# Kernel optimization log

Measured on AMD Instinct MI355X. Metric: run time of the kernel, lower is better.

Reference implementation:

```python
import jax, jax.numpy as jnp
import numpy as np

B, N, ND, H = 8, 1024, 64, 128
NUM_OPS, NUM_PARAMS, SKETCH = 64, 256, 128


def setup_inputs() -> dict:
    key = jax.random.key(0)
    ks = iter(jax.random.split(key, 64))

    def rn(shape, s=0.05):
        return jax.random.normal(next(ks), shape, dtype=jnp.float32) * s

    inp = {
        'node_features': jax.random.normal(next(ks), (B, N, ND), dtype=jnp.float32),
        'adjacency': (jax.random.uniform(next(ks), (B, N, N)) < 0.05).astype(jnp.float32),
        'mask': jnp.ones((B, N), jnp.float32),
    }
    for name, din in (('g1', ND), ('g2', H), ('g3', H)):
        inp[name + '_W'] = rn((din, H))
        inp[name + '_b'] = jnp.zeros((H,), jnp.float32)
        inp[name + '_aW'] = rn((2 * H,))
        inp[name + '_ab'] = jnp.zeros((), jnp.float32)
    for l in (0, 1):
        inp[f'l{l}_Wih'] = rn((4 * H, H))
        inp[f'l{l}_Whh'] = rn((4 * H, H))
        inp[f'l{l}_bih'] = jnp.zeros((4 * H,), jnp.float32)
        inp[f'l{l}_bhh'] = jnp.zeros((4 * H,), jnp.float32)
    for name, dout in (('op', NUM_OPS), ('pa', NUM_PARAMS), ('sk', SKETCH), ('no', ND)):
        inp[name + '_W1'] = rn((H, H))
        inp[name + '_b1'] = jnp.zeros((H,), jnp.float32)
        inp[name + '_W2'] = rn((H, dout))
        inp[name + '_b2'] = jnp.zeros((dout,), jnp.float32)
    return inp


def _gnn(x, adj, W, b, aW, ab):
    # h = Linear(x); att[b,i,j] = sigmoid(aW . [h_j ; h_i] + ab)  (cat order from the torch code)
    h = x @ W + b                      # [B,N,H]
    D = W.shape[1]
    sj = h @ aW[:D]                    # contribution of the dim-1-expanded term (h_j)
    si = h @ aW[D:]                    # contribution of the dim-2-expanded term (h_i)
    att = jax.nn.sigmoid(si[:, :, None] + sj[:, None, :] + ab) * adj  # [B,N,N]
    return jnp.einsum('bij,bjd->bid', att, h)


def _lstm(x, Wih, Whh, bih, bhh):
    # single torch-style LSTM layer, gate order i,f,g,o; zero initial state
    Bx, Hh = x.shape[0], Whh.shape[1]

    def step(carry, xt):
        h, c = carry
        g = xt @ Wih.T + h @ Whh.T + (bih + bhh)       # [B,4H]
        i, f, gg, o = jnp.split(g, 4, axis=-1)
        c = jax.nn.sigmoid(f) * c + jax.nn.sigmoid(i) * jnp.tanh(gg)
        h = jax.nn.sigmoid(o) * jnp.tanh(c)
        return (h, c), h

    z = jnp.zeros((Bx, Hh), x.dtype)
    _, ys = jax.lax.scan(step, (z, z), jnp.swapaxes(x, 0, 1))
    return jnp.swapaxes(ys, 0, 1)


def _mlp(x, W1, b1, W2, b2):
    return jax.nn.relu(x @ W1 + b1) @ W2 + b2


def reference(node_features, adjacency, mask,
              g1_W, g1_b, g1_aW, g1_ab,
              g2_W, g2_b, g2_aW, g2_ab,
              g3_W, g3_b, g3_aW, g3_ab,
              l0_Wih, l0_Whh, l0_bih, l0_bhh,
              l1_Wih, l1_Whh, l1_bih, l1_bhh,
              op_W1, op_b1, op_W2, op_b2,
              pa_W1, pa_b1, pa_W2, pa_b2,
              sk_W1, sk_b1, sk_W2, sk_b2,
              no_W1, no_b1, no_W2, no_b2):
    h = jax.nn.relu(_gnn(node_features, adjacency, g1_W, g1_b, g1_aW, g1_ab))
    h = jax.nn.relu(_gnn(h, adjacency, g2_W, g2_b, g2_aW, g2_ab))
    h = _gnn(h, adjacency, g3_W, g3_b, g3_aW, g3_ab)
    lo = _lstm(h, l0_Wih, l0_Whh, l0_bih, l0_bhh)
    lo = _lstm(lo, l1_Wih, l1_Whh, l1_bih, l1_bhh)
    op_pred = _mlp(lo, op_W1, op_b1, op_W2, op_b2)
    param_pred = _mlp(lo, pa_W1, pa_b1, pa_W2, pa_b2)
    sketch_pred = _mlp(lo, sk_W1, sk_b1, sk_W2, sk_b2)
    node_pred = _mlp(h, no_W1, no_b1, no_W2, no_b2)
    return (op_pred, param_pred, sketch_pred, node_pred)
```

## Files before the change

### kernel.cpp

```cpp
#include <hip/hip_runtime.h>

typedef __attribute__((ext_vector_type(8))) short short8;
typedef __attribute__((ext_vector_type(4))) float f32x4;
typedef __attribute__((ext_vector_type(2))) unsigned int u32x2;

__device__ __forceinline__ unsigned short bf16_of(float f) {
    unsigned u = __builtin_bit_cast(unsigned, f);
    u += 0x7fffu + ((u >> 16) & 1u);
    return (unsigned short)(u >> 16);
}
__device__ __forceinline__ unsigned bf16pk(float a, float b) {
    return (unsigned)bf16_of(a) | ((unsigned)bf16_of(b) << 16);
}
__device__ __forceinline__ float fexp2(float x) { return __builtin_amdgcn_exp2f(x); }
__device__ __forceinline__ float frcp(float x) { return __builtin_amdgcn_rcpf(x); }
__device__ __forceinline__ float sigm(float x) { return frcp(1.f + fexp2(-1.44269504f * x)); }
__device__ __forceinline__ f32x4 mfma16(short8 a, short8 b, f32x4 c) {
    return __builtin_amdgcn_mfma_f32_16x16x32_bf16(a, b, c, 0, 0, 0);
}
__device__ __forceinline__ float dpp_shr8(float x) {
    return __builtin_bit_cast(float, __builtin_amdgcn_update_dpp(
        0, __builtin_bit_cast(int, x), 0x118, 0xF, 0xF, true));
}
__device__ __forceinline__ float dpp_shl8(float x) {
    return __builtin_bit_cast(float, __builtin_amdgcn_update_dpp(
        0, __builtin_bit_cast(int, x), 0x108, 0xF, 0xF, true));
}

__global__ __launch_bounds__(256) void gemm_f32(
    const float* __restrict__ A, const float* __restrict__ B,
    const float* __restrict__ bias, float* __restrict__ C,
    int M, int N, int K, int BT, int RELU, int PACK)
{
    __shared__ float As[64][33];
    __shared__ float Bs[32][68];
    const int tid = threadIdx.x;
    const int tx = tid & 15, ty = tid >> 4;
    const int m0 = blockIdx.y * 64, n0 = blockIdx.x * 64;
    float acc[4][4];
#pragma unroll
    for (int i = 0; i < 4; ++i)
#pragma unroll
        for (int j = 0; j < 4; ++j) acc[i][j] = 0.f;

    for (int k0 = 0; k0 < K; k0 += 32) {
        __syncthreads();
        {
            const int r = tid >> 2, kk = (tid & 3) * 8;
            const float* src = A + (size_t)(m0 + r) * K + k0 + kk;
            f32x4 v0 = *(const f32x4*)src;
            f32x4 v1 = *(const f32x4*)(src + 4);
#pragma unroll
            for (int e = 0; e < 4; ++e) { As[r][kk + e] = v0[e]; As[r][kk + 4 + e] = v1[e]; }
        }
        if (!BT) {
            const int kk = tid >> 3, nn = (tid & 7) * 8;
            const float* src = B + (size_t)(k0 + kk) * N + n0 + nn;
            f32x4 v0 = *(const f32x4*)src;
            f32x4 v1 = *(const f32x4*)(src + 4);
#pragma unroll
            for (int e = 0; e < 4; ++e) { Bs[kk][nn + e] = v0[e]; Bs[kk][nn + 4 + e] = v1[e]; }
        } else {
            const int n = tid >> 2, kk = (tid & 3) * 8;
            const float* src = B + (size_t)(n0 + n) * K + k0 + kk;
            f32x4 v0 = *(const f32x4*)src;
            f32x4 v1 = *(const f32x4*)(src + 4);
#pragma unroll
            for (int e = 0; e < 4; ++e) { Bs[kk + e][n] = v0[e]; Bs[kk + 4 + e][n] = v1[e]; }
        }
        __syncthreads();
#pragma unroll 8
        for (int k = 0; k < 32; ++k) {
            float a0 = As[ty * 4 + 0][k], a1 = As[ty * 4 + 1][k];
            float a2 = As[ty * 4 + 2][k], a3 = As[ty * 4 + 3][k];
            f32x4 bv = *(const f32x4*)&Bs[k][tx * 4];
#pragma unroll
            for (int j = 0; j < 4; ++j) {
                acc[0][j] += a0 * bv[j]; acc[1][j] += a1 * bv[j];
                acc[2][j] += a2 * bv[j]; acc[3][j] += a3 * bv[j];
            }
        }
    }
    f32x4 bv = {};
    if (bias != nullptr) bv = *(const f32x4*)&bias[n0 + tx * 4];
#pragma unroll
    for (int i = 0; i < 4; ++i) {
        f32x4 res = {};
#pragma unroll
        for (int j = 0; j < 4; ++j) {
            float v = acc[i][j] + bv[j];
            if (RELU) v = fmaxf(v, 0.f);
            res[j] = v;
        }
        const int m = m0 + ty * 4 + i;
        if (!PACK) {
            *(f32x4*)&C[(size_t)m * N + n0 + tx * 4] = res;
        } else {
            const int b = m >> 10, t = m & 1023;
            const int n = n0 + tx * 4;
            const int pr = n >> 7, h = n & 127;
            if (pr == 3) {
#pragma unroll
                for (int j = 0; j < 4; ++j) res[j] *= 0.5f;
            }
            *(f32x4*)&C[(((size_t)t * 4 + pr) * 8 + b) * 128 + h] = res;
        }
    }
}

__global__ __launch_bounds__(256) void gemm_gnn(
    const float* __restrict__ A, const float* __restrict__ B,
    const float* __restrict__ bias, const float* __restrict__ aW,
    unsigned short* __restrict__ hT, float* __restrict__ siP,
    float* __restrict__ sjP, int K)
{
    __shared__ float As[64][33];
    __shared__ float Bs[32][68];
    __shared__ unsigned short T[64][70];
    const int tid = threadIdx.x;
    const int tx = tid & 15, ty = tid >> 4;
    const int m0 = blockIdx.y * 64, n0 = blockIdx.x * 64;
    float acc[4][4];
#pragma unroll
    for (int i = 0; i < 4; ++i)
#pragma unroll
        for (int j = 0; j < 4; ++j) acc[i][j] = 0.f;

    for (int k0 = 0; k0 < K; k0 += 32) {
        __syncthreads();
        {
            const int r = tid >> 2, kk = (tid & 3) * 8;
            const float* src = A + (size_t)(m0 + r) * K + k0 + kk;
            f32x4 v0 = *(const f32x4*)src;
            f32x4 v1 = *(const f32x4*)(src + 4);
#pragma unroll
            for (int e = 0; e < 4; ++e) { As[r][kk + e] = v0[e]; As[r][kk + 4 + e] = v1[e]; }
        }
        {
            const int kk = tid >> 3, nn = (tid & 7) * 8;
            const float* src = B + (size_t)(k0 + kk) * 128 + n0 + nn;
            f32x4 v0 = *(const f32x4*)src;
            f32x4 v1 = *(const f32x4*)(src + 4);
#pragma unroll
            for (int e = 0; e < 4; ++e) { Bs[kk][nn + e] = v0[e]; Bs[kk][nn + 4 + e] = v1[e]; }
        }
        __syncthreads();
#pragma unroll 8
        for (int k = 0; k < 32; ++k) {
            float a0 = As[ty * 4 + 0][k], a1 = As[ty * 4 + 1][k];
            float a2 = As[ty * 4 + 2][k], a3 = As[ty * 4 + 3][k];
            f32x4 bv = *(const f32x4*)&Bs[k][tx * 4];
#pragma unroll
            for (int j = 0; j < 4; ++j) {
                acc[0][j] += a0 * bv[j]; acc[1][j] += a1 * bv[j];
                acc[2][j] += a2 * bv[j]; acc[3][j] += a3 * bv[j];
            }
        }
    }
    f32x4 bv = *(const f32x4*)&bias[n0 + tx * 4];
#pragma unroll
    for (int i = 0; i < 4; ++i)
#pragma unroll
        for (int j = 0; j < 4; ++j) acc[i][j] += bv[j];

    f32x4 wj = *(const f32x4*)&aW[n0 + tx * 4];
    f32x4 wi = *(const f32x4*)&aW[128 + n0 + tx * 4];
#pragma unroll
    for (int i = 0; i < 4; ++i) {
        float pj = acc[i][0] * wj[0] + acc[i][1] * wj[1] + acc[i][2] * wj[2] + acc[i][3] * wj[3];
        float pi = acc[i][0] * wi[0] + acc[i][1] * wi[1] + acc[i][2] * wi[2] + acc[i][3] * wi[3];
#pragma unroll
        for (int o = 8; o > 0; o >>= 1) {
            pj += __shfl_xor(pj, o);
            pi += __shfl_xor(pi, o);
        }
        if (tx == 0) {
            const int m = m0 + ty * 4 + i;
            sjP[blockIdx.x * 8192 + m] = pj;
            siP[blockIdx.x * 8192 + m] = pi;
        }
    }

#pragma unroll
    for (int i = 0; i < 4; ++i) {
        unsigned* tp = (unsigned*)&T[ty * 4 + i][tx * 4];
        tp[0] = bf16pk(acc[i][0], acc[i][1]);
        tp[1] = bf16pk(acc[i][2], acc[i][3]);
    }
    __syncthreads();
    const int b = m0 >> 10, node0 = m0 & 1023;
    const int r = tid >> 4, c4 = (tid & 15) * 4;
#pragma unroll
    for (int rr = 0; rr < 4; ++rr) {
        const int d = rr * 16 + r;
        u32x2 o;
        o[0] = (unsigned)T[c4 + 0][d] | ((unsigned)T[c4 + 1][d] << 16);
        o[1] = (unsigned)T[c4 + 2][d] | ((unsigned)T[c4 + 3][d] << 16);
        *(u32x2*)(hT + ((size_t)b * 128 + n0 + d) * 1024 + node0 + c4) = o;
    }
}

__global__ __launch_bounds__(256) void gnn_agg(
    const float* __restrict__ adj, const unsigned short* __restrict__ hT,
    const float* __restrict__ siP, const float* __restrict__ sjP,
    const float* __restrict__ abp, float* __restrict__ out, int RELU)
{
    __shared__ __align__(16) unsigned short Alds[32 * 40];
    __shared__ __align__(16) unsigned short Blds[128 * 40];
    __shared__ float sjL[1024];
    const int b = blockIdx.y, it = blockIdx.x;
    const int i0 = it * 32;
    const int tid = threadIdx.x, lane = tid & 63, w = tid >> 6;
    const int quad = lane >> 4, col = lane & 15;
    const int rh = w & 1, nh = w >> 1;
    const float ab = abp[0];
    const float* adjb = adj + (size_t)b * 1024 * 1024;
    const unsigned short* hTb = hT + (size_t)b * 128 * 1024;

    for (int j = tid; j < 1024; j += 256)
        sjL[j] = sjP[b * 1024 + j] + sjP[8192 + b * 1024 + j];

    const int ar_ = tid >> 3, ash = (tid & 7) * 4;
    const int br_ = tid >> 1, bsh = (tid & 1) * 16;
    const float sii = siP[b * 1024 + i0 + ar_] + siP[8192 + b * 1024 + i0 + ar_] + ab;

    const float* aptr = adjb + (size_t)(i0 + ar_) * 1024 + ash;
    const unsigned short* bptr = hTb + (size_t)br_ * 1024 + bsh;

    f32x4 paA = *(const f32x4*)(aptr);
    short8 pbA0 = *(const short8*)(bptr);
    short8 pbA1 = *(const short8*)(bptr + 8);
    f32x4 paB = *(const f32x4*)(aptr + 32);
    short8 pbB0 = *(const short8*)(bptr + 32);
    short8 pbB1 = *(const short8*)(bptr + 40);

    f32x4 acc[4] = {};

    for (int j0 = 0; j0 < 1024; j0 += 64) {
        __syncthreads();
        {
            float s0 = sigm(sii + sjL[j0 + ash + 0]) * paA[0];
            float s1 = sigm(sii + sjL[j0 + ash + 1]) * paA[1];
            float s2 = sigm(sii + sjL[j0 + ash + 2]) * paA[2];
            float s3 = sigm(sii + sjL[j0 + ash + 3]) * paA[3];
            u32x2 o = {bf16pk(s0, s1), bf16pk(s2, s3)};
            *(u32x2*)&Alds[ar_ * 40 + ash] = o;
            *(short8*)&Blds[br_ * 40 + bsh] = pbA0;
            *(short8*)&Blds[br_ * 40 + bsh + 8] = pbA1;
        }
        if (j0 + 64 < 1024) {
            paA = *(const f32x4*)(aptr + j0 + 64);
            pbA0 = *(const short8*)(bptr + j0 + 64);
            pbA1 = *(const short8*)(bptr + j0 + 72);
        }
        __syncthreads();
        {
            short8 af = *(const short8*)&Alds[(rh * 16 + col) * 40 + quad * 8];
#pragma unroll
            for (int nt = 0; nt < 4; ++nt) {
                short8 bf = *(const short8*)&Blds[((nh * 4 + nt) * 16 + col) * 40 + quad * 8];
                acc[nt] = mfma16(af, bf, acc[nt]);
            }
        }
        __syncthreads();
        {
            float s0 = sigm(sii + sjL[j0 + 32 + ash + 0]) * paB[0];
            float s1 = sigm(sii + sjL[j0 + 32 + ash + 1]) * paB[1];
            float s2 = sigm(sii + sjL[j0 + 32 + ash + 2]) * paB[2];
            float s3 = sigm(sii + sjL[j0 + 32 + ash + 3]) * paB[3];
            u32x2 o = {bf16pk(s0, s1), bf16pk(s2, s3)};
            *(u32x2*)&Alds[ar_ * 40 + ash] = o;
            *(short8*)&Blds[br_ * 40 + bsh] = pbB0;
            *(short8*)&Blds[br_ * 40 + bsh + 8] = pbB1;
        }
        if (j0 + 96 < 1024) {
            paB = *(const f32x4*)(aptr + j0 + 96);
            pbB0 = *(const short8*)(bptr + j0 + 96);
            pbB1 = *(const short8*)(bptr + j0 + 104);
        }
        __syncthreads();
        {
            short8 af = *(const short8*)&Alds[(rh * 16 + col) * 40 + quad * 8];
#pragma unroll
            for (int nt = 0; nt < 4; ++nt) {
                short8 bf = *(const short8*)&Blds[((nh * 4 + nt) * 16 + col) * 40 + quad * 8];
                acc[nt] = mfma16(af, bf, acc[nt]);
            }
        }
    }
    const int ibase = i0 + rh * 16 + quad * 4;
#pragma unroll
    for (int nt = 0; nt < 4; ++nt) {
        const int d = (nh * 4 + nt) * 16 + col;
#pragma unroll
        for (int r = 0; r < 4; ++r) {
            float v = acc[nt][r];
            if (RELU) v = fmaxf(v, 0.f);
            out[((size_t)b * 1024 + ibase + r) * 128 + d] = v;
        }
    }
}

struct PrepArgs {
    const float* src[8];
    unsigned short* dst[8];
    int N[8];
};
__global__ __launch_bounds__(256) void prep_k(
    PrepArgs pa, const float* bih0, const float* bhh0,
    float* bsum, int* flags)
{
    const int m = blockIdx.x;
    const int tid = threadIdx.x;
    if (m < 8) {
        const float* src = pa.src[m];
        unsigned short* dst = pa.dst[m];
        const int N = pa.N[m];
        const int n0 = tid >> 4, kc = (tid & 15) * 8;
        for (int n = n0; n < N; n += 16) {
            unsigned o[4];
#pragma unroll
            for (int e = 0; e < 8; e += 2)
                o[e >> 1] = bf16pk(src[(size_t)(kc + e) * N + n],
                                   src[(size_t)(kc + e + 1) * N + n]);
            *(u32x2*)&dst[n * 128 + kc] = *(u32x2*)&o[0];
            *(u32x2*)&dst[n * 128 + kc + 4] = *(u32x2*)&o[2];
        }
    } else {
        bsum[tid] = bih0[tid] + bhh0[tid];
        bsum[tid + 256] = bih0[tid + 256] + bhh0[tid + 256];
        if (tid < 3) flags[tid] = 0;
    }
}


struct HeadArgs {
    const unsigned short* W1T[4];
    const float* b1[4];
    const unsigned short* W2T[4];
    const float* b2[4];
    float* outp[4];
};

__device__ __forceinline__ void lstm_epilogue(
    const f32x4 accs[4], f32x4 xv0, f32x4 xv1, float* cst, float* hv,
    bool lo, float selLo)
{
    float t0[4], t1[4];
#pragma unroll
    for (int i = 0; i < 4; ++i) {
        float P0 = (lo ? accs[0][i] : dpp_shr8(accs[1][i])) + xv0[i];
        float P1 = (lo ? accs[2][i] : dpp_shr8(accs[3][i])) + xv1[i];
        P1 = fmaxf(P1, -30.f);
        t0[i] = frcp(1.f + fexp2(-1.44269504f * P0));
        float u = fexp2(-2.88539008f * P1);
        t1[i] = (1.f - selLo * u) * frcp(1.f + u);
    }
    float c2[4], og[4];
#pragma unroll
    for (int i = 0; i < 4; ++i) {
        float ig = t0[i];
        float fg = dpp_shl8(t0[i]);
        float gg = t1[i];
        og[i] = dpp_shl8(t1[i]);
        c2[i] = fg * cst[i] + ig * gg;
        cst[i] = c2[i];
    }
    float pc0 = lo ? c2[0] : dpp_shr8(c2[1]);
    float pc1 = lo ? c2[2] : dpp_shr8(c2[3]);
    pc0 = fmaxf(pc0, -30.f);
    pc1 = fmaxf(pc1, -30.f);
    float u0 = fexp2(-2.88539008f * pc0);
    float tc0 = (1.f - u0) * frcp(1.f + u0);
    float u1 = fexp2(-2.88539008f * pc1);
    float tc1 = (1.f - u1) * frcp(1.f + u1);
    float th[4] = {tc0, dpp_shl8(tc0), tc1, dpp_shl8(tc1)};
#pragma unroll
    for (int i = 0; i < 4; ++i) hv[i] = og[i] * th[i];
}

template <int SINK>
__device__ __forceinline__ void lstm_step(
    unsigned short* Hc, unsigned short* Hn, const short8 afr[4][4],
    f32x4 xv0, f32x4 xv1, float* cst, unsigned short* __restrict__ sink,
    int t, int col, int quad, int h4, int b)
{
    short8 bfr[4];
#pragma unroll
    for (int c = 0; c < 4; ++c)
        bfr[c] = *(const short8*)&Hc[col * 136 + c * 32 + quad * 8];
    f32x4 accs[4] = {};
#pragma unroll
    for (int c = 0; c < 4; ++c)
#pragma unroll
        for (int g = 0; g < 4; ++g)
            accs[g] = mfma16(afr[g][c], bfr[c], accs[g]);

    const bool lo = (col < 8);
    const float selLo = lo ? 1.f : 0.f;
    float hv[4];
    lstm_epilogue(accs, xv0, xv1, cst, hv, lo, selLo);
    if (lo) {
        u32x2 hb = {bf16pk(hv[0], hv[1]), bf16pk(hv[2], hv[3])};
        *(u32x2*)&Hn[b * 136 + h4] = hb;
        if (SINK == 0)
            *(u32x2*)(sink + (size_t)t * 1024 + b * 128 + h4) = hb;
        else
            *(u32x2*)(sink + ((size_t)t * 8 + b) * 128 + h4) = hb;
    }
    __builtin_amdgcn_s_waitcnt(0xC07F);
    __builtin_amdgcn_s_barrier();
}

template <int A32, int LROWS>
__device__ void head_strip(
    const void* __restrict__ Asrc, int row0,
    const unsigned short* __restrict__ W1T, const float* __restrict__ b1,
    const unsigned short* __restrict__ W2T, const float* __restrict__ b2,
    float* __restrict__ outp, int dout, unsigned short* A2, int tid)
{
    const int lane = tid & 63, w = tid >> 6;
    const int quad = lane >> 4, col = lane & 15;
    const int mrow = w * 16 + col;
    f32x4 acc[8] = {};
#pragma unroll
    for (int kc = 0; kc < 4; ++kc) {
        short8 af;
        if (A32) {
            const float* s = (const float*)Asrc + (size_t)(row0 + mrow) * 128 + kc * 32 + quad * 8;
            f32x4 v0 = *(const f32x4*)s, v1 = *(const f32x4*)(s + 4);
            short8 v;
#pragma unroll
            for (int j = 0; j < 4; ++j) {
                v[j] = (short)bf16_of(v0[j]);
                v[4 + j] = (short)bf16_of(v1[j]);
            }
            af = v;
        } else {
            af = *(const short8*)((const unsigned short*)Asrc +
                                  (size_t)(row0 + mrow) * 128 + kc * 32 + quad * 8);
        }
#pragma unroll
        for (int nt = 0; nt < 8; ++nt) {
            short8 bf = *(const short8*)&W1T[(nt * 16 + col) * 128 + kc * 32 + quad * 8];
            acc[nt] = mfma16(af, bf, acc[nt]);
        }
    }
    float b1v[8];
#pragma unroll
    for (int nt = 0; nt < 8; ++nt) b1v[nt] = b1[nt * 16 + col];
    __syncthreads();
#pragma unroll
    for (int nt = 0; nt < 8; ++nt)
#pragma unroll
        for (int i = 0; i < 4; ++i) {
            const int mm = w * 16 + quad * 4 + i;
            A2[mm * 136 + nt * 16 + col] = bf16_of(fmaxf(acc[nt][i] + b1v[nt], 0.f));
        }
    __syncthreads();
    const int ntiles = dout >> 4;
    for (int np = 0; np < ntiles; np += 8) {
        const int nts = (ntiles - np < 8) ? ntiles - np : 8;
        f32x4 acc2[8] = {};
#pragma unroll
        for (int kc = 0; kc < 4; ++kc) {
            short8 a2f = *(const short8*)&A2[mrow * 136 + kc * 32 + quad * 8];
            for (int nt = 0; nt < nts; ++nt) {
                short8 bf = *(const short8*)&W2T[((np + nt) * 16 + col) * 128 + kc * 32 + quad * 8];
                acc2[nt] = mfma16(a2f, bf, acc2[nt]);
            }
        }
        for (int nt = 0; nt < nts; ++nt) {
            const int n = (np + nt) * 16 + col;
            const float bb = b2[n];
#pragma unroll
            for (int i = 0; i < 4; ++i) {
                const int r = row0 + w * 16 + quad * 4 + i;
                size_t off;
                if (LROWS) off = ((size_t)(r & 7) * 1024 + (r >> 3)) * dout + n;
                else       off = (size_t)r * dout + n;
                outp[off] = acc2[nt][i] + bb;
            }
        }
    }
}

__global__ __launch_bounds__(512) void lstm_pipe(
    const float* __restrict__ xw0, const float* __restrict__ Whh0,
    const float* __restrict__ Wih1, const float* __restrict__ Whh1,
    const float* __restrict__ bih1, const float* __restrict__ bhh1,
    unsigned short* __restrict__ hbuf, float* __restrict__ xw1,
    int* __restrict__ flags, unsigned short* __restrict__ out1b,
    const float* __restrict__ bufH3, HeadArgs ha)
{
    __shared__ __align__(16) unsigned short H[2][16 * 136];
    __shared__ __align__(16) unsigned short A2[128 * 136];
    const int tid = threadIdx.x;
    const int lane = tid & 63;
    const int w = tid >> 6;
    const int quad = lane >> 4;
    const int col = lane & 15;
    const int b = col & 7;
    const int prA = col >> 3;
    const int h4 = w * 16 + quad * 4;

    if (blockIdx.x >= 3) {
        const int wid = blockIdx.x - 3;
        for (int s = wid; s < 64; s += 8)
            head_strip<1, 0>(bufH3, s * 128, ha.W1T[3], ha.b1[3],
                             ha.W2T[3], ha.b2[3], ha.outp[3], 64, A2, tid);
        for (int s = wid; s < 64; s += 8) {
            if (tid == 0) {
                while (__hip_atomic_load(&flags[2], __ATOMIC_ACQUIRE,
                                         __HIP_MEMORY_SCOPE_AGENT) < s + 1)
                    __builtin_amdgcn_s_sleep(16);
            }
            __syncthreads();
            head_strip<0, 1>(out1b, s * 128, ha.W1T[0], ha.b1[0],
                             ha.W2T[0], ha.b2[0], ha.outp[0], 64, A2, tid);
            head_strip<0, 1>(out1b, s * 128, ha.W1T[1], ha.b1[1],
                             ha.W2T[1], ha.b2[1], ha.outp[1], 256, A2, tid);
            head_strip<0, 1>(out1b, s * 128, ha.W1T[2], ha.b1[2],
                             ha.W2T[2], ha.b2[2], ha.outp[2], 128, A2, tid);
        }
        return;
    }

    if (blockIdx.x == 1) {
        short8 afrI[4][4];
        f32x4 biasv[4];
#pragma unroll
        for (int g = 0; g < 4; ++g) {
            const float gsc = (g == 3) ? 0.5f : 1.f;
            const int row = g * 128 + w * 16 + col;
#pragma unroll
            for (int c = 0; c < 4; ++c) {
                const float* src = Wih1 + row * 128 + c * 32 + quad * 8;
                short8 v;
#pragma unroll
                for (int j = 0; j < 8; ++j) v[j] = (short)bf16_of(src[j] * gsc);
                afrI[g][c] = v;
            }
            const int rb = g * 128 + w * 16 + quad * 4;
            f32x4 b1 = *(const f32x4*)&bih1[rb];
            f32x4 b2 = *(const f32x4*)&bhh1[rb];
#pragma unroll
            for (int e = 0; e < 4; ++e) biasv[g][e] = (b1[e] + b2[e]) * gsc;
        }
        for (int k = 0; k < 64; ++k) {
            if (tid == 0) {
                while (__hip_atomic_load(&flags[0], __ATOMIC_ACQUIRE,
                                         __HIP_MEMORY_SCOPE_AGENT) < k + 1)
                    __builtin_amdgcn_s_sleep(2);
                if (k >= 4) {
                    while (__hip_atomic_load(&flags[2], __ATOMIC_RELAXED,
                                             __HIP_MEMORY_SCOPE_AGENT) < k - 3)
                        __builtin_amdgcn_s_sleep(2);
                }
            }
            __builtin_amdgcn_s_waitcnt(0xC07F);
            __builtin_amdgcn_s_barrier();
            const unsigned short* hb = hbuf + (size_t)k * 16 * 1024;
            float* dst = xw1 + (size_t)(k & 3) * 65536;
#pragma unroll 2
            for (int nt = 0; nt < 8; ++nt) {
                const int tl = nt * 2 + (col >> 3);
                const unsigned short* src = hb + tl * 1024 + b * 128 + quad * 8;
                short8 bfr[4];
#pragma unroll
                for (int c = 0; c < 4; ++c) bfr[c] = *(const short8*)&src[c * 32];
                f32x4 acc[4] = {};
#pragma unroll
                for (int c = 0; c < 4; ++c)
#pragma unroll
                    for (int g = 0; g < 4; ++g)
                        acc[g] = mfma16(afrI[g][c], bfr[c], acc[g]);
#pragma unroll
                for (int g = 0; g < 4; ++g) {
                    f32x4 res;
#pragma unroll
                    for (int e = 0; e < 4; ++e) res[e] = acc[g][e] + biasv[g][e];
                    *(f32x4*)&dst[((tl * 4 + g) * 8 + b) * 128 + w * 16 + quad * 4] = res;
                }
            }
            __builtin_amdgcn_s_waitcnt(0x0F70);
            __builtin_amdgcn_s_barrier();
            if (tid == 0)
                __hip_atomic_store(&flags[1], k + 1, __ATOMIC_RELEASE,
                                   __HIP_MEMORY_SCOPE_AGENT);
        }
        return;
    }

    for (int i = tid; i < 2 * 16 * 136; i += 512) (&H[0][0])[i] = 0;
    float cst[4] = {0.f, 0.f, 0.f, 0.f};
    const int lane_off = (prA * 8 + b) * 128 + h4;

    if (blockIdx.x == 0) {
        short8 afr[4][4];
#pragma unroll
        for (int g = 0; g < 4; ++g) {
            const float gsc = (g == 3) ? 0.5f : 1.f;
            const int row = g * 128 + w * 16 + col;
#pragma unroll
            for (int c = 0; c < 4; ++c) {
                const float* src = Whh0 + row * 128 + c * 32 + quad * 8;
                short8 v;
#pragma unroll
                for (int j = 0; j < 8; ++j) v[j] = (short)bf16_of(src[j] * gsc);
                afr[g][c] = v;
            }
        }
        const float* xp = xw0 + lane_off;
        f32x4 p0a = *(const f32x4*)(xp);
        f32x4 p1a = *(const f32x4*)(xp + 2048);
        f32x4 p0b = *(const f32x4*)(xp + 4096);
        f32x4 p1b = *(const f32x4*)(xp + 6144);
        xp += 8192;
        __syncthreads();

        for (int t = 0; t < 1024; t += 2) {
            const float* xr = (t == 1022) ? xp - 8192 : xp;
            {
                f32x4 xv0 = p0a, xv1 = p1a;
                p0a = *(const f32x4*)(xr);
                p1a = *(const f32x4*)(xr + 2048);
                lstm_step<0>(&H[0][0], &H[1][0], afr, xv0, xv1, cst, hbuf, t, col, quad, h4, b);
            }
            {
                f32x4 xv0 = p0b, xv1 = p1b;
                p0b = *(const f32x4*)(xr + 4096);
                p1b = *(const f32x4*)(xr + 6144);
                lstm_step<0>(&H[1][0], &H[0][0], afr, xv0, xv1, cst, hbuf, t + 1, col, quad, h4, b);
            }
            xp += 8192;
            if ((t & 14) == 14) {
                __syncthreads();
                if (tid == 0)
                    __hip_atomic_store(&flags[0], (t >> 4) + 1, __ATOMIC_RELEASE,
                                       __HIP_MEMORY_SCOPE_AGENT);
            }
        }
    } else {
        short8 afr[4][4];
#pragma unroll
        for (int g = 0; g < 4; ++g) {
            const float gsc = (g == 3) ? 0.5f : 1.f;
            const int row = g * 128 + w * 16 + col;
#pragma unroll
            for (int c = 0; c < 4; ++c) {
                const float* src = Whh1 + row * 128 + c * 32 + quad * 8;
                short8 v;
#pragma unroll
                for (int j = 0; j < 8; ++j) v[j] = (short)bf16_of(src[j] * gsc);
                afr[g][c] = v;
            }
        }
        __syncthreads();
        auto xaddr = [&](int t) -> const float* {
            return xw1 + (((t >> 4) & 3) * 65536 + (t & 15) * 4096) + lane_off;
        };
        while (__hip_atomic_load(&flags[1], __ATOMIC_ACQUIRE,
                                 __HIP_MEMORY_SCOPE_AGENT) < 2)
            __builtin_amdgcn_s_sleep(2);
        f32x4 p0a = *(const f32x4*)xaddr(0);
        f32x4 p1a = *(const f32x4*)(xaddr(0) + 2048);
        f32x4 p0b = *(const f32x4*)xaddr(1);
        f32x4 p1b = *(const f32x4*)(xaddr(1) + 2048);

        for (int c = 0; c < 64; ++c) {
            if (c > 0) {
                const int target = (c + 2 < 64) ? c + 2 : 64;
                if (tid == 0) {
                    while (__hip_atomic_load(&flags[1], __ATOMIC_ACQUIRE,
                                             __HIP_MEMORY_SCOPE_AGENT) < target)
                        __builtin_amdgcn_s_sleep(2);
                }
                __builtin_amdgcn_s_waitcnt(0xC07F);
                __builtin_amdgcn_s_barrier();
            }
            for (int s = 0; s < 16; s += 2) {
                const int t = c * 16 + s;
                const int t2 = (t + 2 < 1024) ? t + 2 : 1023;
                const int t3 = (t + 3 < 1024) ? t + 3 : 1023;
                {
                    f32x4 xv0 = p0a, xv1 = p1a;
                    p0a = *(const f32x4*)xaddr(t2);
                    p1a = *(const f32x4*)(xaddr(t2) + 2048);
                    lstm_step<1>(&H[0][0], &H[1][0], afr, xv0, xv1, cst, out1b, t, col, quad, h4, b);
                }
                {
                    f32x4 xv0 = p0b, xv1 = p1b;
                    p0b = *(const f32x4*)xaddr(t3);
                    p1b = *(const f32x4*)(xaddr(t3) + 2048);
                    lstm_step<1>(&H[1][0], &H[0][0], afr, xv0, xv1, cst, out1b, t + 1, col, quad, h4, b);
                }
            }
            __syncthreads();
            if (tid == 0)
                __hip_atomic_store(&flags[2], c + 1, __ATOMIC_RELEASE,
                                   __HIP_MEMORY_SCOPE_AGENT);
        }
    }
}

extern "C" void kernel_launch(void* const* d_in, const int* in_sizes, int n_in,
                              void* d_out, int out_size, void* d_ws, size_t ws_size,
                              hipStream_t stream)
{
    (void)in_sizes; (void)n_in; (void)out_size; (void)ws_size;
    const float* nf    = (const float*)d_in[0];
    const float* adj   = (const float*)d_in[1];
    const float* g1W   = (const float*)d_in[3];
    const float* g1b   = (const float*)d_in[4];
    const float* g1aW  = (const float*)d_in[5];
    const float* g1ab  = (const float*)d_in[6];
    const float* g2W   = (const float*)d_in[7];
    const float* g2b   = (const float*)d_in[8];
    const float* g2aW  = (const float*)d_in[9];
    const float* g2ab  = (const float*)d_in[10];
    const float* g3W   = (const float*)d_in[11];
    const float* g3b   = (const float*)d_in[12];
    const float* g3aW  = (const float*)d_in[13];
    const float* g3ab  = (const float*)d_in[14];
    const float* l0Wih = (const float*)d_in[15];
    const float* l0Whh = (const float*)d_in[16];
    const float* l0bih = (const float*)d_in[17];
    const float* l0bhh = (const float*)d_in[18];
    const float* l1Wih = (const float*)d_in[19];
    const float* l1Whh = (const float*)d_in[20];
    const float* l1bih = (const float*)d_in[21];
    const float* l1bhh = (const float*)d_in[22];
    const float* opW1 = (const float*)d_in[23];
    const float* opb1 = (const float*)d_in[24];
    const float* opW2 = (const float*)d_in[25];
    const float* opb2 = (const float*)d_in[26];
    const float* paW1 = (const float*)d_in[27];
    const float* pab1 = (const float*)d_in[28];
    const float* paW2 = (const float*)d_in[29];
    const float* pab2 = (const float*)d_in[30];
    const float* skW1 = (const float*)d_in[31];
    const float* skb1 = (const float*)d_in[32];
    const float* skW2 = (const float*)d_in[33];
    const float* skb2 = (const float*)d_in[34];
    const float* noW1 = (const float*)d_in[35];
    const float* nob1 = (const float*)d_in[36];
    const float* noW2 = (const float*)d_in[37];
    const float* nob2 = (const float*)d_in[38];

    float* out = (float*)d_out;
    float* ws = (float*)d_ws;
    float* siP   = ws;
    float* sjP   = ws + 16384;
    float* bufX  = ws + 1048576;
    float* bufH3 = ws + 2097152;
    unsigned short* bufT = (unsigned short*)(ws + 3145728);
    float* bsum = ws + 3686400;
    float* xw0  = ws + 3687424;
    float* xw1  = ws + 7881728;
    int*  flags = (int*)(ws + 8143872);
    unsigned short* WT = (unsigned short*)(ws + 8143876);
    unsigned short* out1b = (unsigned short*)(ws + 8209412);
    unsigned short* hbuf = (unsigned short*)bufX;

    unsigned short* opW1T = WT;
    unsigned short* paW1T = WT + 16384;
    unsigned short* skW1T = WT + 32768;
    unsigned short* noW1T = WT + 49152;
    unsigned short* opW2T = WT + 65536;
    unsigned short* paW2T = WT + 73728;
    unsigned short* skW2T = WT + 106496;
    unsigned short* noW2T = WT + 122880;

    gemm_gnn<<<dim3(2, 128), 256, 0, stream>>>(nf, g1W, g1b, g1aW, bufT, siP, sjP, 64);
    gnn_agg<<<dim3(32, 8), 256, 0, stream>>>(adj, bufT, siP, sjP, g1ab, bufX, 1);
    gemm_gnn<<<dim3(2, 128), 256, 0, stream>>>(bufX, g2W, g2b, g2aW, bufT, siP, sjP, 128);
    gnn_agg<<<dim3(32, 8), 256, 0, stream>>>(adj, bufT, siP, sjP, g2ab, bufX, 1);
    gemm_gnn<<<dim3(2, 128), 256, 0, stream>>>(bufX, g3W, g3b, g3aW, bufT, siP, sjP, 128);
    gnn_agg<<<dim3(32, 8), 256, 0, stream>>>(adj, bufT, siP, sjP, g3ab, bufH3, 0);

    PrepArgs pargs;
    pargs.src[0] = opW1; pargs.dst[0] = opW1T; pargs.N[0] = 128;
    pargs.src[1] = paW1; pargs.dst[1] = paW1T; pargs.N[1] = 128;
    pargs.src[2] = skW1; pargs.dst[2] = skW1T; pargs.N[2] = 128;
    pargs.src[3] = noW1; pargs.dst[3] = noW1T; pargs.N[3] = 128;
    pargs.src[4] = opW2; pargs.dst[4] = opW2T; pargs.N[4] = 64;
    pargs.src[5] = paW2; pargs.dst[5] = paW2T; pargs.N[5] = 256;
    pargs.src[6] = skW2; pargs.dst[6] = skW2T; pargs.N[6] = 128;
    pargs.src[7] = noW2; pargs.dst[7] = noW2T; pargs.N[7] = 64;
    prep_k<<<9, 256, 0, stream>>>(pargs, l0bih, l0bhh, bsum, flags);

    {
        dim3 g(512 / 64, 8192 / 64);
        gemm_f32<<<g, dim3(256), 0, stream>>>(bufH3, l0Wih, bsum, xw0,
                                              8192, 512, 128, 1, 0, 1);
    }

    HeadArgs ha;
    ha.W1T[0] = opW1T; ha.b1[0] = opb1; ha.W2T[0] = opW2T; ha.b2[0] = opb2;
    ha.outp[0] = out + 0;
    ha.W1T[1] = paW1T; ha.b1[1] = pab1; ha.W2T[1] = paW2T; ha.b2[1] = pab2;
    ha.outp[1] = out + 524288;
    ha.W1T[2] = skW1T; ha.b1[2] = skb1; ha.W2T[2] = skW2T; ha.b2[2] = skb2;
    ha.outp[2] = out + 2621440;
    ha.W1T[3] = noW1T; ha.b1[3] = nob1; ha.W2T[3] = noW2T; ha.b2[3] = nob2;
    ha.outp[3] = out + 3670016;
    lstm_pipe<<<11, 512, 0, stream>>>(xw0, l0Whh, l1Wih, l1Whh, l1bih, l1bhh,
                                      hbuf, xw1, flags, out1b, bufH3, ha);
}
```

Measured before the change: 1.346 ms.

## Run both LSTM layer recurrences interleaved in one block with shared barriers

The layer-0 and layer-1 recurrences, previously on separate blocks, now run in a single block. Layer 1 trails layer 0 by 48 steps, and the two steps are interleaved so one barrier per step pair covers both layers, hiding each step's MFMA and epilogue latency behind the other's. This doubles the resident recurrent weight fragments in registers (launch bounds changed to 512,2), and the block count drops by one. The risks are register pressure or spills, a longer dependent chain per step, and a more fragile flag handshake with the Wih1 projection block.

```diff
diff --git a/kernel.cpp b/kernel.cpp
--- a/kernel.cpp
+++ b/kernel.cpp
@@ -379,9 +379,9 @@
     for (int i = 0; i < 4; ++i) hv[i] = og[i] * th[i];
 }
 
-template <int SINK>
+template <int SINK, int BAR>
 __device__ __forceinline__ void lstm_step(
-    unsigned short* Hc, unsigned short* Hn, const short8 afr[4][4],
+    const unsigned short* Hc, unsigned short* Hn, const short8 afr[4][4],
     f32x4 xv0, f32x4 xv1, float* cst, unsigned short* __restrict__ sink,
     int t, int col, int quad, int h4, int b)
 {
@@ -408,8 +408,10 @@
         else
             *(u32x2*)(sink + ((size_t)t * 8 + b) * 128 + h4) = hb;
     }
-    __builtin_amdgcn_s_waitcnt(0xC07F);
-    __builtin_amdgcn_s_barrier();
+    if (BAR) {
+        __builtin_amdgcn_s_waitcnt(0xC07F);
+        __builtin_amdgcn_s_barrier();
+    }
 }
 
 template <int A32, int LROWS>
@@ -485,7 +487,7 @@
     }
 }
 
-__global__ __launch_bounds__(512) void lstm_pipe(
+__global__ __launch_bounds__(512, 2) void lstm_pipe(
     const float* __restrict__ xw0, const float* __restrict__ Whh0,
     const float* __restrict__ Wih1, const float* __restrict__ Whh1,
     const float* __restrict__ bih1, const float* __restrict__ bhh1,
@@ -493,7 +495,7 @@
     int* __restrict__ flags, unsigned short* __restrict__ out1b,
     const float* __restrict__ bufH3, HeadArgs ha)
 {
-    __shared__ __align__(16) unsigned short H[2][16 * 136];
+    __shared__ __align__(16) unsigned short H[4][16 * 136];
     __shared__ __align__(16) unsigned short A2[128 * 136];
     const int tid = threadIdx.x;
     const int lane = tid & 63;
@@ -504,8 +506,8 @@
     const int prA = col >> 3;
     const int h4 = w * 16 + quad * 4;
 
-    if (blockIdx.x >= 3) {
-        const int wid = blockIdx.x - 3;
+    if (blockIdx.x >= 2) {
+        const int wid = blockIdx.x - 2;
         for (int s = wid; s < 64; s += 8)
             head_strip<1, 0>(bufH3, s * 128, ha.W1T[3], ha.b1[3],
                              ha.W2T[3], ha.b2[3], ha.outp[3], 64, A2, tid);
@@ -592,113 +594,153 @@
         return;
     }
 
-    for (int i = tid; i < 2 * 16 * 136; i += 512) (&H[0][0])[i] = 0;
-    float cst[4] = {0.f, 0.f, 0.f, 0.f};
+    for (int i = tid; i < 4 * 16 * 136; i += 512) (&H[0][0])[i] = 0;
+    float cst0[4] = {0.f, 0.f, 0.f, 0.f};
+    float cst1[4] = {0.f, 0.f, 0.f, 0.f};
     const int lane_off = (prA * 8 + b) * 128 + h4;
 
-    if (blockIdx.x == 0) {
-        short8 afr[4][4];
-#pragma unroll
-        for (int g = 0; g < 4; ++g) {
-            const float gsc = (g == 3) ? 0.5f : 1.f;
-            const int row = g * 128 + w * 16 + col;
-#pragma unroll
-            for (int c = 0; c < 4; ++c) {
-                const float* src = Whh0 + row * 128 + c * 32 + quad * 8;
-                short8 v;
-#pragma unroll
-                for (int j = 0; j < 8; ++j) v[j] = (short)bf16_of(src[j] * gsc);
-                afr[g][c] = v;
-            }
-        }
-        const float* xp = xw0 + lane_off;
-        f32x4 p0a = *(const f32x4*)(xp);
-        f32x4 p1a = *(const f32x4*)(xp + 2048);
-        f32x4 p0b = *(const f32x4*)(xp + 4096);
-        f32x4 p1b = *(const f32x4*)(xp + 6144);
+    short8 afr0[4][4], afr1[4][4];
+#pragma unroll
+    for (int g = 0; g < 4; ++g) {
+        const float gsc = (g == 3) ? 0.5f : 1.f;
+        const int row = g * 128 + w * 16 + col;
+#pragma unroll
+        for (int c = 0; c < 4; ++c) {
+            const float* s0 = Whh0 + row * 128 + c * 32 + quad * 8;
+            const float* s1 = Whh1 + row * 128 + c * 32 + quad * 8;
+            short8 v0, v1;
+#pragma unroll
+            for (int j = 0; j < 8; ++j) {
+                v0[j] = (short)bf16_of(s0[j] * gsc);
+                v1[j] = (short)bf16_of(s1[j] * gsc);
+            }
+            afr0[g][c] = v0;
+            afr1[g][c] = v1;
+        }
+    }
+
+    const float* xp = xw0 + lane_off;
+    f32x4 q0a = *(const f32x4*)(xp);
+    f32x4 q1a = *(const f32x4*)(xp + 2048);
+    f32x4 q0b = *(const f32x4*)(xp + 4096);
+    f32x4 q1b = *(const f32x4*)(xp + 6144);
+    xp += 8192;
+    __syncthreads();
+
+    for (int t = 0; t < 48; t += 2) {
+        {
+            f32x4 xv0 = q0a, xv1 = q1a;
+            q0a = *(const f32x4*)(xp);
+            q1a = *(const f32x4*)(xp + 2048);
+            lstm_step<0, 1>(&H[0][0], &H[1][0], afr0, xv0, xv1, cst0, hbuf, t, col, quad, h4, b);
+        }
+        {
+            f32x4 xv0 = q0b, xv1 = q1b;
+            q0b = *(const f32x4*)(xp + 4096);
+            q1b = *(const f32x4*)(xp + 6144);
+            lstm_step<0, 1>(&H[1][0], &H[0][0], afr0, xv0, xv1, cst0, hbuf, t + 1, col, quad, h4, b);
+        }
         xp += 8192;
-        __syncthreads();
-
-        for (int t = 0; t < 1024; t += 2) {
-            const float* xr = (t == 1022) ? xp - 8192 : xp;
-            {
-                f32x4 xv0 = p0a, xv1 = p1a;
-                p0a = *(const f32x4*)(xr);
-                p1a = *(const f32x4*)(xr + 2048);
-                lstm_step<0>(&H[0][0], &H[1][0], afr, xv0, xv1, cst, hbuf, t, col, quad, h4, b);
-            }
-            {
-                f32x4 xv0 = p0b, xv1 = p1b;
-                p0b = *(const f32x4*)(xr + 4096);
-                p1b = *(const f32x4*)(xr + 6144);
-                lstm_step<0>(&H[1][0], &H[0][0], afr, xv0, xv1, cst, hbuf, t + 1, col, quad, h4, b);
-            }
-            xp += 8192;
-            if ((t & 14) == 14) {
-                __syncthreads();
-                if (tid == 0)
-                    __hip_atomic_store(&flags[0], (t >> 4) + 1, __ATOMIC_RELEASE,
-                                       __HIP_MEMORY_SCOPE_AGENT);
-            }
-        }
-    } else {
-        short8 afr[4][4];
-#pragma unroll
-        for (int g = 0; g < 4; ++g) {
-            const float gsc = (g == 3) ? 0.5f : 1.f;
-            const int row = g * 128 + w * 16 + col;
-#pragma unroll
-            for (int c = 0; c < 4; ++c) {
-                const float* src = Whh1 + row * 128 + c * 32 + quad * 8;
-                short8 v;
-#pragma unroll
-                for (int j = 0; j < 8; ++j) v[j] = (short)bf16_of(src[j] * gsc);
-                afr[g][c] = v;
-            }
-        }
-        __syncthreads();
-        auto xaddr = [&](int t) -> const float* {
-            return xw1 + (((t >> 4) & 3) * 65536 + (t & 15) * 4096) + lane_off;
-        };
+        if ((t & 14) == 14) {
+            __syncthreads();
+            if (tid == 0)
+                __hip_atomic_store(&flags[0], (t >> 4) + 1, __ATOMIC_RELEASE,
+                                   __HIP_MEMORY_SCOPE_AGENT);
+        }
+    }
+
+    auto xaddr = [&](int t) -> const float* {
+        return xw1 + (((t >> 4) & 3) * 65536 + (t & 15) * 4096) + lane_off;
+    };
+    if (tid == 0) {
         while (__hip_atomic_load(&flags[1], __ATOMIC_ACQUIRE,
                                  __HIP_MEMORY_SCOPE_AGENT) < 2)
             __builtin_amdgcn_s_sleep(2);
-        f32x4 p0a = *(const f32x4*)xaddr(0);
-        f32x4 p1a = *(const f32x4*)(xaddr(0) + 2048);
-        f32x4 p0b = *(const f32x4*)xaddr(1);
-        f32x4 p1b = *(const f32x4*)(xaddr(1) + 2048);
-
-        for (int c = 0; c < 64; ++c) {
-            if (c > 0) {
-                const int target = (c + 2 < 64) ? c + 2 : 64;
-                if (tid == 0) {
-                    while (__hip_atomic_load(&flags[1], __ATOMIC_ACQUIRE,
-                                             __HIP_MEMORY_SCOPE_AGENT) < target)
-                        __builtin_amdgcn_s_sleep(2);
-                }
-                __builtin_amdgcn_s_waitcnt(0xC07F);
-                __builtin_amdgcn_s_barrier();
-            }
-            for (int s = 0; s < 16; s += 2) {
-                const int t = c * 16 + s;
-                const int t2 = (t + 2 < 1024) ? t + 2 : 1023;
-                const int t3 = (t + 3 < 1024) ? t + 3 : 1023;
-                {
-                    f32x4 xv0 = p0a, xv1 = p1a;
-                    p0a = *(const f32x4*)xaddr(t2);
-                    p1a = *(const f32x4*)(xaddr(t2) + 2048);
-                    lstm_step<1>(&H[0][0], &H[1][0], afr, xv0, xv1, cst, out1b, t, col, quad, h4, b);
-                }
-                {
-                    f32x4 xv0 = p0b, xv1 = p1b;
-                    p0b = *(const f32x4*)xaddr(t3);
-                    p1b = *(const f32x4*)(xaddr(t3) + 2048);
-                    lstm_step<1>(&H[1][0], &H[0][0], afr, xv0, xv1, cst, out1b, t + 1, col, quad, h4, b);
-                }
-            }
+    }
+    __builtin_amdgcn_s_waitcnt(0xC07F);
+    __builtin_amdgcn_s_barrier();
+    f32x4 r0a = *(const f32x4*)xaddr(0);
+    f32x4 r1a = *(const f32x4*)(xaddr(0) + 2048);
+    f32x4 r0b = *(const f32x4*)xaddr(1);
+    f32x4 r1b = *(const f32x4*)(xaddr(1) + 2048);
+
+    for (int t = 48; t < 1024; t += 2) {
+        const int tc = t - 48;
+        if (tc > 0 && (tc & 15) == 0) {
+            const int c = tc >> 4;
+            const int target = (c + 2 < 64) ? c + 2 : 64;
+            if (tid == 0) {
+                while (__hip_atomic_load(&flags[1], __ATOMIC_ACQUIRE,
+                                         __HIP_MEMORY_SCOPE_AGENT) < target)
+                    __builtin_amdgcn_s_sleep(2);
+            }
+            __builtin_amdgcn_s_waitcnt(0xC07F);
+            __builtin_amdgcn_s_barrier();
+        }
+        const float* xr = (t == 1022) ? xp - 8192 : xp;
+        {
+            f32x4 xv0 = q0a, xv1 = q1a;
+            q0a = *(const f32x4*)(xr);
+            q1a = *(const f32x4*)(xr + 2048);
+            lstm_step<0, 0>(&H[0][0], &H[1][0], afr0, xv0, xv1, cst0, hbuf, t, col, quad, h4, b);
+            f32x4 yv0 = r0a, yv1 = r1a;
+            r0a = *(const f32x4*)xaddr(tc + 2);
+            r1a = *(const f32x4*)(xaddr(tc + 2) + 2048);
+            lstm_step<1, 1>(&H[2][0], &H[3][0], afr1, yv0, yv1, cst1, out1b, tc, col, quad, h4, b);
+        }
+        {
+            f32x4 xv0 = q0b, xv1 = q1b;
+            q0b = *(const f32x4*)(xr + 4096);
+            q1b = *(const f32x4*)(xr + 6144);
+            lstm_step<0, 0>(&H[1][0], &H[0][0], afr0, xv0, xv1, cst0, hbuf, t + 1, col, quad, h4, b);
+            f32x4 yv0 = r0b, yv1 = r1b;
+            r0b = *(const f32x4*)xaddr(tc + 3);
+            r1b = *(const f32x4*)(xaddr(tc + 3) + 2048);
+            lstm_step<1, 1>(&H[3][0], &H[2][0], afr1, yv0, yv1, cst1, out1b, tc + 1, col, quad, h4, b);
+        }
+        xp += 8192;
+        if ((t & 14) == 14) {
+            __syncthreads();
+            if (tid == 0) {
+                __hip_atomic_store(&flags[0], (t >> 4) + 1, __ATOMIC_RELEASE,
+                                   __HIP_MEMORY_SCOPE_AGENT);
+                __hip_atomic_store(&flags[2], (tc >> 4) + 1, __ATOMIC_RELEASE,
+                                   __HIP_MEMORY_SCOPE_AGENT);
+            }
+        }
+    }
+
+    for (int t = 1024; t < 1072; t += 2) {
+        const int tc = t - 48;
+        if ((tc & 15) == 0) {
+            const int c = tc >> 4;
+            const int target = (c + 2 < 64) ? c + 2 : 64;
+            if (tid == 0) {
+                while (__hip_atomic_load(&flags[1], __ATOMIC_ACQUIRE,
+                                         __HIP_MEMORY_SCOPE_AGENT) < target)
+                    __builtin_amdgcn_s_sleep(2);
+            }
+            __builtin_amdgcn_s_waitcnt(0xC07F);
+            __builtin_amdgcn_s_barrier();
+        }
+        const int t2 = (tc + 2 < 1024) ? tc + 2 : 1023;
+        const int t3 = (tc + 3 < 1024) ? tc + 3 : 1023;
+        {
+            f32x4 yv0 = r0a, yv1 = r1a;
+            r0a = *(const f32x4*)xaddr(t2);
+            r1a = *(const f32x4*)(xaddr(t2) + 2048);
+            lstm_step<1, 1>(&H[2][0], &H[3][0], afr1, yv0, yv1, cst1, out1b, tc, col, quad, h4, b);
+        }
+        {
+            f32x4 yv0 = r0b, yv1 = r1b;
+            r0b = *(const f32x4*)xaddr(t3);
+            r1b = *(const f32x4*)(xaddr(t3) + 2048);
+            lstm_step<1, 1>(&H[3][0], &H[2][0], afr1, yv0, yv1, cst1, out1b, tc + 1, col, quad, h4, b);
+        }
+        if ((tc & 14) == 14) {
             __syncthreads();
             if (tid == 0)
-                __hip_atomic_store(&flags[2], c + 1, __ATOMIC_RELEASE,
+                __hip_atomic_store(&flags[2], (tc >> 4) + 1, __ATOMIC_RELEASE,
                                    __HIP_MEMORY_SCOPE_AGENT);
         }
     }
@@ -805,6 +847,6 @@
     ha.outp[2] = out + 2621440;
     ha.W1T[3] = noW1T; ha.b1[3] = nob1; ha.W2T[3] = noW2T; ha.b2[3] = nob2;
     ha.outp[3] = out + 3670016;
-    lstm_pipe<<<11, 512, 0, stream>>>(xw0, l0Whh, l1Wih, l1Whh, l1bih, l1bhh,
+    lstm_pipe<<<10, 512, 0, stream>>>(xw0, l0Whh, l1Wih, l1Whh, l1bih, l1bhh,
                                       hbuf, xw1, flags, out1b, bufH3, ha);
 }
```

Result: slower. 2.170 ms (+61.2%).

## Halve LSTM recurrence waves, each computing two 16-row hidden strips

Applied to the files above, without the earlier changes.

The two recurrent LSTM blocks now run with 4 active waves instead of 8. Each wave holds Whh fragments for two 16-row hidden strips and issues 32 MFMAs per step instead of 16. The aim is a cheaper per-step block barrier and fewer waves contending for the shared H buffer on the serial critical path. The cost is more serial MFMA and epilogue work per wave, plus double the register footprint for weights, which the new launch bound of 2 may pressure.

```diff
diff --git a/kernel.cpp b/kernel.cpp
--- a/kernel.cpp
+++ b/kernel.cpp
@@ -380,33 +380,40 @@
 }
 
 template <int SINK>
-__device__ __forceinline__ void lstm_step(
-    unsigned short* Hc, unsigned short* Hn, const short8 afr[4][4],
-    f32x4 xv0, f32x4 xv1, float* cst, unsigned short* __restrict__ sink,
-    int t, int col, int quad, int h4, int b)
+__device__ __forceinline__ void lstm_step2(
+    const unsigned short* Hc, unsigned short* Hn, const short8 afr[4][2][4],
+    const f32x4 xv0[2], const f32x4 xv1[2], float cst[2][4],
+    unsigned short* __restrict__ sink,
+    int t, int col, int quad, int w, int b)
 {
     short8 bfr[4];
 #pragma unroll
     for (int c = 0; c < 4; ++c)
         bfr[c] = *(const short8*)&Hc[col * 136 + c * 32 + quad * 8];
-    f32x4 accs[4] = {};
+    f32x4 accs[2][4] = {};
 #pragma unroll
     for (int c = 0; c < 4; ++c)
 #pragma unroll
-        for (int g = 0; g < 4; ++g)
-            accs[g] = mfma16(afr[g][c], bfr[c], accs[g]);
+        for (int st = 0; st < 2; ++st)
+#pragma unroll
+            for (int g = 0; g < 4; ++g)
+                accs[st][g] = mfma16(afr[g][st][c], bfr[c], accs[st][g]);
 
     const bool lo = (col < 8);
     const float selLo = lo ? 1.f : 0.f;
-    float hv[4];
-    lstm_epilogue(accs, xv0, xv1, cst, hv, lo, selLo);
-    if (lo) {
-        u32x2 hb = {bf16pk(hv[0], hv[1]), bf16pk(hv[2], hv[3])};
-        *(u32x2*)&Hn[b * 136 + h4] = hb;
-        if (SINK == 0)
-            *(u32x2*)(sink + (size_t)t * 1024 + b * 128 + h4) = hb;
-        else
-            *(u32x2*)(sink + ((size_t)t * 8 + b) * 128 + h4) = hb;
+#pragma unroll
+    for (int st = 0; st < 2; ++st) {
+        float hv[4];
+        lstm_epilogue(accs[st], xv0[st], xv1[st], cst[st], hv, lo, selLo);
+        const int h4 = w * 32 + st * 16 + quad * 4;
+        if (lo) {
+            u32x2 hb = {bf16pk(hv[0], hv[1]), bf16pk(hv[2], hv[3])};
+            *(u32x2*)&Hn[b * 136 + h4] = hb;
+            if (SINK == 0)
+                *(u32x2*)(sink + (size_t)t * 1024 + b * 128 + h4) = hb;
+            else
+                *(u32x2*)(sink + ((size_t)t * 8 + b) * 128 + h4) = hb;
+        }
     }
     __builtin_amdgcn_s_waitcnt(0xC07F);
     __builtin_amdgcn_s_barrier();
@@ -485,7 +492,7 @@
     }
 }
 
-__global__ __launch_bounds__(512) void lstm_pipe(
+__global__ __launch_bounds__(512, 2) void lstm_pipe(
     const float* __restrict__ xw0, const float* __restrict__ Whh0,
     const float* __restrict__ Wih1, const float* __restrict__ Whh1,
     const float* __restrict__ bih1, const float* __restrict__ bhh1,
@@ -502,7 +509,6 @@
     const int col = lane & 15;
     const int b = col & 7;
     const int prA = col >> 3;
-    const int h4 = w * 16 + quad * 4;
 
     if (blockIdx.x >= 3) {
         const int wid = blockIdx.x - 3;
@@ -592,46 +598,64 @@
         return;
     }
 
-    for (int i = tid; i < 2 * 16 * 136; i += 512) (&H[0][0])[i] = 0;
-    float cst[4] = {0.f, 0.f, 0.f, 0.f};
-    const int lane_off = (prA * 8 + b) * 128 + h4;
+    if (w >= 4) return;
+
+    for (int i = tid; i < 2 * 16 * 136; i += 256) (&H[0][0])[i] = 0;
+    float cst[2][4] = {};
+    int lofs[2];
+#pragma unroll
+    for (int st = 0; st < 2; ++st)
+        lofs[st] = (prA * 8 + b) * 128 + w * 32 + st * 16 + quad * 4;
 
     if (blockIdx.x == 0) {
-        short8 afr[4][4];
+        short8 afr[4][2][4];
 #pragma unroll
         for (int g = 0; g < 4; ++g) {
             const float gsc = (g == 3) ? 0.5f : 1.f;
-            const int row = g * 128 + w * 16 + col;
-#pragma unroll
-            for (int c = 0; c < 4; ++c) {
-                const float* src = Whh0 + row * 128 + c * 32 + quad * 8;
-                short8 v;
-#pragma unroll
-                for (int j = 0; j < 8; ++j) v[j] = (short)bf16_of(src[j] * gsc);
-                afr[g][c] = v;
-            }
-        }
-        const float* xp = xw0 + lane_off;
-        f32x4 p0a = *(const f32x4*)(xp);
-        f32x4 p1a = *(const f32x4*)(xp + 2048);
-        f32x4 p0b = *(const f32x4*)(xp + 4096);
-        f32x4 p1b = *(const f32x4*)(xp + 6144);
+#pragma unroll
+            for (int st = 0; st < 2; ++st) {
+                const int row = g * 128 + w * 32 + st * 16 + col;
+#pragma unroll
+                for (int c = 0; c < 4; ++c) {
+                    const float* src = Whh0 + row * 128 + c * 32 + quad * 8;
+                    short8 v;
+#pragma unroll
+                    for (int j = 0; j < 8; ++j) v[j] = (short)bf16_of(src[j] * gsc);
+                    afr[g][st][c] = v;
+                }
+            }
+        }
+        const float* xp = xw0;
+        f32x4 p0a[2], p1a[2], p0b[2], p1b[2];
+#pragma unroll
+        for (int st = 0; st < 2; ++st) {
+            p0a[st] = *(const f32x4*)(xp + lofs[st]);
+            p1a[st] = *(const f32x4*)(xp + lofs[st] + 2048);
+            p0b[st] = *(const f32x4*)(xp + lofs[st] + 4096);
+            p1b[st] = *(const f32x4*)(xp + lofs[st] + 6144);
+        }
         xp += 8192;
         __syncthreads();
 
         for (int t = 0; t < 1024; t += 2) {
             const float* xr = (t == 1022) ? xp - 8192 : xp;
             {
-                f32x4 xv0 = p0a, xv1 = p1a;
-                p0a = *(const f32x4*)(xr);
-                p1a = *(const f32x4*)(xr + 2048);
-                lstm_step<0>(&H[0][0], &H[1][0], afr, xv0, xv1, cst, hbuf, t, col, quad, h4, b);
+                f32x4 xv0[2] = {p0a[0], p0a[1]}, xv1[2] = {p1a[0], p1a[1]};
+#pragma unroll
+                for (int st = 0; st < 2; ++st) {
+                    p0a[st] = *(const f32x4*)(xr + lofs[st]);
+                    p1a[st] = *(const f32x4*)(xr + lofs[st] + 2048);
+                }
+                lstm_step2<0>(&H[0][0], &H[1][0], afr, xv0, xv1, cst, hbuf, t, col, quad, w, b);
             }
             {
-                f32x4 xv0 = p0b, xv1 = p1b;
-                p0b = *(const f32x4*)(xr + 4096);
-                p1b = *(const f32x4*)(xr + 6144);
-                lstm_step<0>(&H[1][0], &H[0][0], afr, xv0, xv1, cst, hbuf, t + 1, col, quad, h4, b);
+                f32x4 xv0[2] = {p0b[0], p0b[1]}, xv1[2] = {p1b[0], p1b[1]};
+#pragma unroll
+                for (int st = 0; st < 2; ++st) {
+                    p0b[st] = *(const f32x4*)(xr + lofs[st] + 4096);
+                    p1b[st] = *(const f32x4*)(xr + lofs[st] + 6144);
+                }
+                lstm_step2<0>(&H[1][0], &H[0][0], afr, xv0, xv1, cst, hbuf, t + 1, col, quad, w, b);
             }
             xp += 8192;
             if ((t & 14) == 14) {
@@ -642,31 +666,38 @@
             }
         }
     } else {
-        short8 afr[4][4];
+        short8 afr[4][2][4];
 #pragma unroll
         for (int g = 0; g < 4; ++g) {
             const float gsc = (g == 3) ? 0.5f : 1.f;
-            const int row = g * 128 + w * 16 + col;
-#pragma unroll
-            for (int c = 0; c < 4; ++c) {
-                const float* src = Whh1 + row * 128 + c * 32 + quad * 8;
-                short8 v;
-#pragma unroll
-                for (int j = 0; j < 8; ++j) v[j] = (short)bf16_of(src[j] * gsc);
-                afr[g][c] = v;
-            }
-        }
-        __syncthreads();
-        auto xaddr = [&](int t) -> const float* {
-            return xw1 + (((t >> 4) & 3) * 65536 + (t & 15) * 4096) + lane_off;
+#pragma unroll
+            for (int st = 0; st < 2; ++st) {
+                const int row = g * 128 + w * 32 + st * 16 + col;
+#pragma unroll
+                for (int c = 0; c < 4; ++c) {
+                    const float* src = Whh1 + row * 128 + c * 32 + quad * 8;
+                    short8 v;
+#pragma unroll
+                    for (int j = 0; j < 8; ++j) v[j] = (short)bf16_of(src[j] * gsc);
+                    afr[g][st][c] = v;
+                }
+            }
+        }
+        __syncthreads();
+        auto xbase = [&](int t) -> const float* {
+            return xw1 + (((t >> 4) & 3) * 65536 + (t & 15) * 4096);
         };
         while (__hip_atomic_load(&flags[1], __ATOMIC_ACQUIRE,
                                  __HIP_MEMORY_SCOPE_AGENT) < 2)
             __builtin_amdgcn_s_sleep(2);
-        f32x4 p0a = *(const f32x4*)xaddr(0);
-        f32x4 p1a = *(const f32x4*)(xaddr(0) + 2048);
-        f32x4 p0b = *(const f32x4*)xaddr(1);
-        f32x4 p1b = *(const f32x4*)(xaddr(1) + 2048);
+        f32x4 r0a[2], r1a[2], r0b[2], r1b[2];
+#pragma unroll
+        for (int st = 0; st < 2; ++st) {
+            r0a[st] = *(const f32x4*)(xbase(0) + lofs[st]);
+            r1a[st] = *(const f32x4*)(xbase(0) + lofs[st] + 2048);
+            r0b[st] = *(const f32x4*)(xbase(1) + lofs[st]);
+            r1b[st] = *(const f32x4*)(xbase(1) + lofs[st] + 2048);
+        }
 
         for (int c = 0; c < 64; ++c) {
             if (c > 0) {
@@ -684,16 +715,22 @@
                 const int t2 = (t + 2 < 1024) ? t + 2 : 1023;
                 const int t3 = (t + 3 < 1024) ? t + 3 : 1023;
                 {
-                    f32x4 xv0 = p0a, xv1 = p1a;
-                    p0a = *(const f32x4*)xaddr(t2);
-                    p1a = *(const f32x4*)(xaddr(t2) + 2048);
-                    lstm_step<1>(&H[0][0], &H[1][0], afr, xv0, xv1, cst, out1b, t, col, quad, h4, b);
+                    f32x4 xv0[2] = {r0a[0], r0a[1]}, xv1[2] = {r1a[0], r1a[1]};
+#pragma unroll
+                    for (int st = 0; st < 2; ++st) {
+                        r0a[st] = *(const f32x4*)(xbase(t2) + lofs[st]);
+                        r1a[st] = *(const f32x4*)(xbase(t2) + lofs[st] + 2048);
+                    }
+                    lstm_step2<1>(&H[0][0], &H[1][0], afr, xv0, xv1, cst, out1b, t, col, quad, w, b);
                 }
                 {
-                    f32x4 xv0 = p0b, xv1 = p1b;
-                    p0b = *(const f32x4*)xaddr(t3);
-                    p1b = *(const f32x4*)(xaddr(t3) + 2048);
-                    lstm_step<1>(&H[1][0], &H[0][0], afr, xv0, xv1, cst, out1b, t + 1, col, quad, h4, b);
+                    f32x4 xv0[2] = {r0b[0], r0b[1]}, xv1[2] = {r1b[0], r1b[1]};
+#pragma unroll
+                    for (int st = 0; st < 2; ++st) {
+                        r0b[st] = *(const f32x4*)(xbase(t3) + lofs[st]);
+                        r1b[st] = *(const f32x4*)(xbase(t3) + lofs[st] + 2048);
+                    }
+                    lstm_step2<1>(&H[1][0], &H[0][0], afr, xv0, xv1, cst, out1b, t + 1, col, quad, w, b);
                 }
             }
             __syncthreads();
```

Measured after the change: 1.527 ms. 13.4% more time.
